# Kernel tuning notes

Hardware: AMD Instinct MI355X
Metric: run time of the kernel (lower is better)

## Reference

```python
import jax, jax.numpy as jnp
import numpy as np

N = 100_000
E = 1_600_000
F_IN, D1, D2, D_EMB = 64, 32, 64, 64
NUM_GRAPHS = 16
BN_EPS = 1e-5


def _glorot(key, shape):
    fan_in, fan_out = shape[0], shape[1]
    lim = (6.0 / (fan_in + fan_out)) ** 0.5
    return jax.random.uniform(key, shape, jnp.float32, -lim, lim)


def setup_inputs() -> dict:
    key = jax.random.key(0)
    ks = jax.random.split(key, 12)
    x = jax.random.normal(ks[0], (N, F_IN), jnp.float32)
    edge_index = jax.random.randint(ks[1], (2, E), 0, N, jnp.int64)
    batch = jnp.sort(jax.random.randint(ks[2], (N,), 0, NUM_GRAPHS, jnp.int64))
    return {
        "x": x,
        "edge_index": edge_index,
        "batch": batch,
        "num_graphs": NUM_GRAPHS,
        "num_nodes": N,
        "W1a": _glorot(ks[3], (F_IN, D1)), "b1a": jnp.zeros((D1,), jnp.float32),
        "W1b": _glorot(ks[4], (D1, D2)), "b1b": jnp.zeros((D2,), jnp.float32),
        "g1": jnp.ones((D2,), jnp.float32), "be1": jnp.zeros((D2,), jnp.float32),
        "W2a": _glorot(ks[5], (D2, D2)), "b2a": jnp.zeros((D2,), jnp.float32),
        "W2b": _glorot(ks[6], (D2, D_EMB)), "b2b": jnp.zeros((D_EMB,), jnp.float32),
        "g2": jnp.ones((D_EMB,), jnp.float32), "be2": jnp.zeros((D_EMB,), jnp.float32),
    }


def _batchnorm_train(h, gamma, beta):
    mean = jnp.mean(h, axis=0)
    var = jnp.mean(jnp.square(h - mean), axis=0)  # biased var, as torch BN uses for normalization
    return (h - mean) * jax.lax.rsqrt(var + BN_EPS) * gamma + beta


def _gin_aggregate(x, src, dst, valid, n_nodes):
    # sum_{j in N(i)} x_j over valid edges only (masked scatter-add)
    msg = x[src] * valid[:, None]  # [E, D]
    return jax.ops.segment_sum(msg, dst, num_segments=n_nodes)


def reference(x, edge_index, batch, num_graphs, num_nodes,
              W1a, b1a, W1b, b1b, g1, be1,
              W2a, b2a, W2b, b2b, g2, be2):
    n_edges = edge_index.shape[1]
    per = n_edges // num_graphs
    # edge_mask: per-edge threshold g * num_nodes / num_graphs applied to both rows
    thresh = jnp.repeat(jnp.arange(num_graphs), per).astype(jnp.float32) * (num_nodes / num_graphs)
    valid = jnp.all(edge_index.astype(jnp.float32) - thresh[None, :] >= 0.0, axis=0)
    valid = valid.astype(x.dtype)
    src, dst = edge_index[0], edge_index[1]

    # GINConv 1 (eps=0): nn1(x + aggr)
    h = x + _gin_aggregate(x, src, dst, valid, num_nodes)
    h = jax.nn.relu(h @ W1a + b1a) @ W1b + b1b
    h = jax.nn.relu(h)
    h = _batchnorm_train(h, g1, be1)

    # GINConv 2
    h = h + _gin_aggregate(h, src, dst, valid, num_nodes)
    h = jax.nn.relu(h @ W2a + b2a) @ W2b + b2b
    h = jax.nn.relu(h)
    h = _batchnorm_train(h, g2, be2)

    # global_mean_pool
    sums = jax.ops.segment_sum(h, batch, num_segments=num_graphs)
    counts = jax.ops.segment_sum(jnp.ones((h.shape[0],), h.dtype), batch, num_segments=num_graphs)
    return sums / jnp.maximum(counts, 1.0)[:, None]
```

## Files before the change

kernel.cpp:

```cpp
#include <hip/hip_runtime.h>
#include <hip/hip_fp16.h>

#define NG 16
#define D 64
#define SLOT 32
#define INP 68
#define NPB 64

union HF4 { float4 f4; __half2 h2[4]; };
union HF2 { float2 f2; __half2 h2[2]; };

__global__ void to_half_kernel(const float* __restrict__ in,
                               float2* __restrict__ out, int n4,
                               float4* __restrict__ xz,
                               float4* __restrict__ hz) {
  int t = blockIdx.x * 256 + threadIdx.x;
  if (blockIdx.x == 0 && threadIdx.x < 16) {
    float4 z = make_float4(0.f, 0.f, 0.f, 0.f);
    if (threadIdx.x < 8) xz[threadIdx.x] = z;
    else hz[threadIdx.x - 8] = z;
  }
  if (t < n4) {
    float4 v = ((const float4*)in)[t];
    HF2 u;
    u.h2[0] = __floats2half2_rn(v.x, v.y);
    u.h2[1] = __floats2half2_rn(v.z, v.w);
    out[t] = u.f2;
  }
}

__global__ void build_csr_kernel(const int* __restrict__ ei,
                                 int* __restrict__ fill,
                                 int* __restrict__ col,
                                 int E, int per, int tmul) {
  int e = blockIdx.x * blockDim.x + threadIdx.x;
  if (e >= E) return;
  int src = ei[e];
  int dst = ei[E + e];
  int g = e / per;
  int thr = g * tmul;
  if (src >= thr && dst >= thr) {
    int k = atomicAdd(&fill[dst], 1);
    if (k < SLOT) col[dst * SLOT + k] = src;
  }
}

__device__ __forceinline__ void tree_reduce_2x32(float* s_in, int tid) {
#pragma unroll
  for (int s = 16; s >= 1; s >>= 1) {
    if (tid < 32 * s) {
      int h = tid / (16 * s);
      int r = (tid / 16) % s;
      int qq = tid & 15;
      float4* a = (float4*)&s_in[(h * 32 + r) * INP + qq * 4];
      const float4 b = *(const float4*)&s_in[(h * 32 + r + s) * INP + qq * 4];
      a->x += b.x; a->y += b.y; a->z += b.z; a->w += b.w;
    }
    __syncthreads();
  }
}

template <int MID, bool FOLD_BN, int EPI>
__global__ __launch_bounds__(512, 2) void fused_layer_kernel(
    const float4* __restrict__ feat4,
    const int* __restrict__ col, const int* __restrict__ deg,
    const float* __restrict__ bn_sum, const float* __restrict__ bn_sq,
    const float* __restrict__ bn_gamma, const float* __restrict__ bn_beta,
    float invN,
    const float* __restrict__ Wa, const float* __restrict__ ba,
    const float* __restrict__ Wb, const float* __restrict__ bb,
    float2* __restrict__ out2,
    const int* __restrict__ batch,
    float* __restrict__ st_sum,
    float* __restrict__ st_sq,
    float* __restrict__ cnt,
    int N) {
  __shared__ float s_in[NPB * INP];
  __shared__ __half s_Wa[D * MID];
  __shared__ __half s_Wb[MID * D];
  __shared__ float s_bna[FOLD_BN ? D : 1];
  __shared__ float s_bnb[FOLD_BN ? D : 1];
  __shared__ int s_cnt[2];

  int tid = threadIdx.x;

  {
    const float4* wa4 = (const float4*)Wa;
    const float4* wb4 = (const float4*)Wb;
    __half2* sa2 = (__half2*)s_Wa;
    __half2* sb2 = (__half2*)s_Wb;
    constexpr int NW = D * MID / 4;
#pragma unroll
    for (int i = tid; i < NW; i += 512) {
      float4 a = wa4[i];
      float4 b = wb4[i];
      sa2[2 * i + 0] = __floats2half2_rn(a.x, a.y);
      sa2[2 * i + 1] = __floats2half2_rn(a.z, a.w);
      sb2[2 * i + 0] = __floats2half2_rn(b.x, b.y);
      sb2[2 * i + 1] = __floats2half2_rn(b.z, b.w);
    }
  }
  if (FOLD_BN && tid < D) {
    float mean = bn_sum[tid] * invN;
    float var = bn_sq[tid] * invN - mean * mean;
    float av = bn_gamma[tid] * rsqrtf(var + 1e-5f);
    s_bna[tid] = av;
    s_bnb[tid] = bn_beta[tid] - mean * av;
  }
  if (EPI == 2 && tid < 2) s_cnt[tid] = 0;
  __syncthreads();

  int base = blockIdx.x * NPB;

  {
    int slot = tid >> 3;
    int q8 = tid & 7;
    int node = base + slot;
    if (node < N) {
      int d = min(deg[node], SLOT);
      const int* cl = col + node * SLOT;
      float acc[8];
      {
        HF4 s; s.f4 = feat4[(size_t)node * 8 + q8];
#pragma unroll
        for (int i = 0; i < 4; i++) {
          float2 f = __half22float2(s.h2[i]);
          acc[2 * i] = f.x; acc[2 * i + 1] = f.y;
        }
      }
      int dpad = (d + 7) & ~7;
      for (int j = 0; j < dpad; j += 8) {
        int4 sa = *(const int4*)(cl + j);
        int4 sb = *(const int4*)(cl + j + 4);
        int i0 = (j + 0 < d) ? sa.x : N;
        int i1 = (j + 1 < d) ? sa.y : N;
        int i2 = (j + 2 < d) ? sa.z : N;
        int i3 = (j + 3 < d) ? sa.w : N;
        int i4 = (j + 4 < d) ? sb.x : N;
        int i5 = (j + 5 < d) ? sb.y : N;
        int i6 = (j + 6 < d) ? sb.z : N;
        int i7 = (j + 7 < d) ? sb.w : N;
        HF4 u0, u1, u2, u3, u4, u5, u6, u7;
        u0.f4 = feat4[(size_t)i0 * 8 + q8];
        u1.f4 = feat4[(size_t)i1 * 8 + q8];
        u2.f4 = feat4[(size_t)i2 * 8 + q8];
        u3.f4 = feat4[(size_t)i3 * 8 + q8];
        u4.f4 = feat4[(size_t)i4 * 8 + q8];
        u5.f4 = feat4[(size_t)i5 * 8 + q8];
        u6.f4 = feat4[(size_t)i6 * 8 + q8];
        u7.f4 = feat4[(size_t)i7 * 8 + q8];
#pragma unroll
        for (int i = 0; i < 4; i++) {
          float2 f0 = __half22float2(u0.h2[i]), f1 = __half22float2(u1.h2[i]);
          float2 f2 = __half22float2(u2.h2[i]), f3 = __half22float2(u3.h2[i]);
          float2 f4 = __half22float2(u4.h2[i]), f5 = __half22float2(u5.h2[i]);
          float2 f6 = __half22float2(u6.h2[i]), f7 = __half22float2(u7.h2[i]);
          acc[2 * i]     += (f0.x + f1.x + f2.x + f3.x) + (f4.x + f5.x + f6.x + f7.x);
          acc[2 * i + 1] += (f0.y + f1.y + f2.y + f3.y) + (f4.y + f5.y + f6.y + f7.y);
        }
      }
      if (FOLD_BN) {
        float dp = (float)(d + 1);
        int c = q8 * 8;
#pragma unroll
        for (int i = 0; i < 8; i++)
          acc[i] = s_bna[c + i] * acc[i] + dp * s_bnb[c + i];
      }
      *(float4*)&s_in[slot * INP + q8 * 8] =
          make_float4(acc[0], acc[1], acc[2], acc[3]);
      *(float4*)&s_in[slot * INP + q8 * 8 + 4] =
          make_float4(acc[4], acc[5], acc[6], acc[7]);
    }
  }
  __syncthreads();

  int q = tid & 15;
  int r2 = tid >> 4;
  int n0 = 2 * r2, n1 = n0 + 1;
  int node0 = base + n0, node1 = base + n1;
  constexpr int C1 = MID / 16;
  float4 o0, o1;
  {
    float acc0[C1], acc1[C1];
#pragma unroll
    for (int u = 0; u < C1; u++) { acc0[u] = ba[q * C1 + u]; acc1[u] = acc0[u]; }
#pragma unroll 4
    for (int j = 0; j < D; j++) {
      float v0 = s_in[n0 * INP + j];
      float v1 = s_in[n1 * INP + j];
      if constexpr (C1 == 2) {
        float2 w = __half22float2(((const __half2*)s_Wa)[j * 16 + q]);
        acc0[0] += v0 * w.x; acc0[1] += v0 * w.y;
        acc1[0] += v1 * w.x; acc1[1] += v1 * w.y;
      } else {
        HF2 u; u.f2 = ((const float2*)s_Wa)[j * 16 + q];
        float2 wA = __half22float2(u.h2[0]);
        float2 wB = __half22float2(u.h2[1]);
        acc0[0] += v0 * wA.x; acc0[1] += v0 * wA.y;
        acc0[2] += v0 * wB.x; acc0[3] += v0 * wB.y;
        acc1[0] += v1 * wA.x; acc1[1] += v1 * wA.y;
        acc1[2] += v1 * wB.x; acc1[3] += v1 * wB.y;
      }
    }
#pragma unroll
    for (int u = 0; u < C1; u++) {
      acc0[u] = fmaxf(acc0[u], 0.f);
      acc1[u] = fmaxf(acc1[u], 0.f);
    }

    o0 = *(const float4*)(bb + q * 4);
    o1 = o0;
#pragma unroll 8
    for (int k = 0; k < MID; k++) {
      float m0 = __shfl(acc0[k % C1], k / C1, 16);
      float m1 = __shfl(acc1[k % C1], k / C1, 16);
      HF2 u; u.f2 = ((const float2*)s_Wb)[k * 16 + q];
      float2 wA = __half22float2(u.h2[0]);
      float2 wB = __half22float2(u.h2[1]);
      o0.x += m0 * wA.x; o0.y += m0 * wA.y; o0.z += m0 * wB.x; o0.w += m0 * wB.y;
      o1.x += m1 * wA.x; o1.y += m1 * wA.y; o1.z += m1 * wB.x; o1.w += m1 * wB.y;
    }
    o0.x = fmaxf(o0.x, 0.f); o0.y = fmaxf(o0.y, 0.f);
    o0.z = fmaxf(o0.z, 0.f); o0.w = fmaxf(o0.w, 0.f);
    o1.x = fmaxf(o1.x, 0.f); o1.y = fmaxf(o1.y, 0.f);
    o1.z = fmaxf(o1.z, 0.f); o1.w = fmaxf(o1.w, 0.f);
    if (EPI == 1) {
      if (node0 < N) {
        HF2 u;
        u.h2[0] = __floats2half2_rn(o0.x, o0.y);
        u.h2[1] = __floats2half2_rn(o0.z, o0.w);
        out2[(size_t)node0 * 16 + q] = u.f2;
      }
      if (node1 < N) {
        HF2 u;
        u.h2[0] = __floats2half2_rn(o1.x, o1.y);
        u.h2[1] = __floats2half2_rn(o1.z, o1.w);
        out2[(size_t)node1 * 16 + q] = u.f2;
      }
    }
    if (node0 >= N) o0 = make_float4(0.f, 0.f, 0.f, 0.f);
    if (node1 >= N) o1 = make_float4(0.f, 0.f, 0.f, 0.f);
  }

  if (EPI == 1) {
    __syncthreads();
    *(float4*)&s_in[r2 * INP + q * 4] =
        make_float4(o0.x + o1.x, o0.y + o1.y, o0.z + o1.z, o0.w + o1.w);
    *(float4*)&s_in[(32 + r2) * INP + q * 4] =
        make_float4(o0.x * o0.x + o1.x * o1.x, o0.y * o0.y + o1.y * o1.y,
                    o0.z * o0.z + o1.z * o1.z, o0.w * o0.w + o1.w * o1.w);
    __syncthreads();
    tree_reduce_2x32(s_in, tid);
    if (tid < D) {
      atomicAdd(&st_sum[tid], s_in[tid]);
      atomicAdd(&st_sq[tid], s_in[32 * INP + tid]);
    }
  }

  if (EPI == 2) {
    int b0 = (node0 < N) ? batch[node0] : -1;
    int b1 = (node1 < N) ? batch[node1] : -1;
    int g_lo = batch[base];
    int g_hi = batch[min(base + NPB - 1, N - 1)];

    __syncthreads();
    if (q == 0) {
      atomicAdd(&s_cnt[0], (b0 == g_lo ? 1 : 0) + (b1 == g_lo ? 1 : 0));
      if (g_hi != g_lo)
        atomicAdd(&s_cnt[1], (b0 == g_hi ? 1 : 0) + (b1 == g_hi ? 1 : 0));
    }

    float w0 = (b0 == g_lo) ? 1.f : 0.f;
    float w1 = (b1 == g_lo) ? 1.f : 0.f;
    *(float4*)&s_in[r2 * INP + q * 4] =
        make_float4(w0 * o0.x + w1 * o1.x, w0 * o0.y + w1 * o1.y,
                    w0 * o0.z + w1 * o1.z, w0 * o0.w + w1 * o1.w);
    *(float4*)&s_in[(32 + r2) * INP + q * 4] =
        make_float4(o0.x * o0.x + o1.x * o1.x, o0.y * o0.y + o1.y * o1.y,
                    o0.z * o0.z + o1.z * o1.z, o0.w * o0.w + o1.w * o1.w);
    __syncthreads();
    tree_reduce_2x32(s_in, tid);
    if (tid < D) {
      atomicAdd(&st_sum[g_lo * D + tid], s_in[tid]);
      atomicAdd(&st_sq[tid], s_in[32 * INP + tid]);
    }
    if (tid == 0) atomicAdd(&cnt[g_lo], (float)s_cnt[0]);

    if (g_hi != g_lo) {
      __syncthreads();
      float u0 = (b0 == g_hi) ? 1.f : 0.f;
      float u1 = (b1 == g_hi) ? 1.f : 0.f;
      *(float4*)&s_in[r2 * INP + q * 4] =
          make_float4(u0 * o0.x + u1 * o1.x, u0 * o0.y + u1 * o1.y,
                      u0 * o0.z + u1 * o1.z, u0 * o0.w + u1 * o1.w);
      *(float4*)&s_in[(32 + r2) * INP + q * 4] = make_float4(0.f, 0.f, 0.f, 0.f);
      __syncthreads();
      tree_reduce_2x32(s_in, tid);
      if (tid < D) atomicAdd(&st_sum[g_hi * D + tid], s_in[tid]);
      if (tid == 0) atomicAdd(&cnt[g_hi], (float)s_cnt[1]);
    }
  }
}

__global__ void final_kernel(const float* __restrict__ pool,
                             const float* __restrict__ cnt,
                             const float* __restrict__ sq,
                             const float* __restrict__ gamma,
                             const float* __restrict__ beta,
                             float invN, float* __restrict__ out) {
  int c = threadIdx.x;
  float s = 0.f;
#pragma unroll
  for (int g = 0; g < NG; g++) s += pool[g * D + c];
  float mean = s * invN;
  float var = sq[c] * invN - mean * mean;
  float a = gamma[c] * rsqrtf(var + 1e-5f);
  float b = beta[c] - mean * a;
#pragma unroll
  for (int g = 0; g < NG; g++) {
    float n = cnt[g];
    out[g * D + c] = (a * pool[g * D + c] + n * b) / fmaxf(n, 1.f);
  }
}

extern "C" void kernel_launch(void* const* d_in, const int* in_sizes, int n_in,
                              void* d_out, int out_size, void* d_ws, size_t ws_size,
                              hipStream_t stream) {
  const float* x   = (const float*)d_in[0];
  const int* ei    = (const int*)d_in[1];
  const int* batch = (const int*)d_in[2];
  const float* W1a = (const float*)d_in[5];
  const float* b1a = (const float*)d_in[6];
  const float* W1b = (const float*)d_in[7];
  const float* b1b = (const float*)d_in[8];
  const float* g1  = (const float*)d_in[9];
  const float* be1 = (const float*)d_in[10];
  const float* W2a = (const float*)d_in[11];
  const float* b2a = (const float*)d_in[12];
  const float* W2b = (const float*)d_in[13];
  const float* b2b = (const float*)d_in[14];
  const float* g2  = (const float*)d_in[15];
  const float* be2 = (const float*)d_in[16];

  int N = in_sizes[0] / D;
  int E = in_sizes[1] / 2;
  int per = E / NG;
  int tmul = N / NG;
  float invN = 1.f / (float)N;

  float* ws = (float*)d_ws;
  size_t ndh = (size_t)(N + 1) * D / 2;
  float* h1h = ws;
  float* xh  = ws + ndh;
  int*   col = (int*)(ws + 2 * ndh);
  float* stats = ws + 2 * ndh + (size_t)N * SLOT;
  float* sum1 = stats;
  float* sq1  = stats + 64;
  float* pool = stats + 128;
  float* cnt  = stats + 128 + NG * D;
  float* sq2  = stats + 144 + NG * D;
  int*   fill = (int*)(stats + 208 + NG * D);

  hipMemsetAsync(stats, 0, (208 + NG * D + N) * sizeof(float), stream);

  int n4 = N * D / 4;
  to_half_kernel<<<(n4 + 255) / 256, 256, 0, stream>>>(
      x, (float2*)xh, n4,
      (float4*)(xh + (size_t)N * D / 2),
      (float4*)(h1h + (size_t)N * D / 2));

  build_csr_kernel<<<(E + 255) / 256, 256, 0, stream>>>(ei, fill, col, E, per, tmul);

  int fblocks = (N + NPB - 1) / NPB;

  fused_layer_kernel<32, false, 1><<<fblocks, 512, 0, stream>>>(
      (const float4*)xh, col, fill, nullptr, nullptr, nullptr, nullptr, invN,
      W1a, b1a, W1b, b1b, (float2*)h1h, nullptr, sum1, sq1, nullptr, N);

  fused_layer_kernel<64, true, 2><<<fblocks, 512, 0, stream>>>(
      (const float4*)h1h, col, fill, sum1, sq1, g1, be1, invN,
      W2a, b2a, W2b, b2b, nullptr, batch, pool, sq2, cnt, N);

  final_kernel<<<1, 64, 0, stream>>>(pool, cnt, sq2, g2, be2, invN, (float*)d_out);
}
```

Measured before the change: 264.3 us.

## Merge all stages into one persistent cooperative kernel with grid syncs

Replaces the memset, half conversion, CSR build, two fused layer kernels and the final kernel with a single cooperative launch that separates phases with grid.sync(). Blocks are persistent and loop over node tiles, and weights are staged into shared memory once per block per layer instead of once per tile. The goal is to remove per-launch overhead and the gaps between kernels. The cost is grid-wide barriers, a host-side occupancy query on every call, a grid limited to the resident block count, and shared memory now sized for the larger layer.

```diff
diff --git a/kernel.cpp b/kernel.cpp
--- a/kernel.cpp
+++ b/kernel.cpp
@@ -1,5 +1,8 @@
 #include <hip/hip_runtime.h>
 #include <hip/hip_fp16.h>
+#include <hip/hip_cooperative_groups.h>
+
+namespace cg = cooperative_groups;
 
 #define NG 16
 #define D 64
@@ -10,40 +13,19 @@
 union HF4 { float4 f4; __half2 h2[4]; };
 union HF2 { float2 f2; __half2 h2[2]; };
 
-__global__ void to_half_kernel(const float* __restrict__ in,
-                               float2* __restrict__ out, int n4,
-                               float4* __restrict__ xz,
-                               float4* __restrict__ hz) {
-  int t = blockIdx.x * 256 + threadIdx.x;
-  if (blockIdx.x == 0 && threadIdx.x < 16) {
-    float4 z = make_float4(0.f, 0.f, 0.f, 0.f);
-    if (threadIdx.x < 8) xz[threadIdx.x] = z;
-    else hz[threadIdx.x - 8] = z;
-  }
-  if (t < n4) {
-    float4 v = ((const float4*)in)[t];
-    HF2 u;
-    u.h2[0] = __floats2half2_rn(v.x, v.y);
-    u.h2[1] = __floats2half2_rn(v.z, v.w);
-    out[t] = u.f2;
-  }
-}
-
-__global__ void build_csr_kernel(const int* __restrict__ ei,
-                                 int* __restrict__ fill,
-                                 int* __restrict__ col,
-                                 int E, int per, int tmul) {
-  int e = blockIdx.x * blockDim.x + threadIdx.x;
-  if (e >= E) return;
-  int src = ei[e];
-  int dst = ei[E + e];
-  int g = e / per;
-  int thr = g * tmul;
-  if (src >= thr && dst >= thr) {
-    int k = atomicAdd(&fill[dst], 1);
-    if (k < SLOT) col[dst * SLOT + k] = src;
-  }
-}
+struct Params {
+  const float* x; const int* ei; const int* batch;
+  const float* W1a; const float* b1a; const float* W1b; const float* b1b;
+  const float* g1; const float* be1;
+  const float* W2a; const float* b2a; const float* W2b; const float* b2b;
+  const float* g2; const float* be2;
+  float* h1h; float* xh; int* col;
+  float* sum1; float* sq1; float* pool; float* cnt; float* sq2; int* fill;
+  int* zero_base; int zero_n;
+  float* out;
+  int N, E, per, tmul, n4, ntiles;
+  float invN;
+};
 
 __device__ __forceinline__ void tree_reduce_2x32(float* s_in, int tid) {
 #pragma unroll
@@ -60,57 +42,38 @@
   }
 }
 
+template <int MID>
+__device__ __forceinline__ void stage_weights(__half* s_Wa, __half* s_Wb,
+                                              const float* Wa, const float* Wb,
+                                              int tid) {
+  const float4* wa4 = (const float4*)Wa;
+  const float4* wb4 = (const float4*)Wb;
+  __half2* sa2 = (__half2*)s_Wa;
+  __half2* sb2 = (__half2*)s_Wb;
+  constexpr int NW = D * MID / 4;
+#pragma unroll
+  for (int i = tid; i < NW; i += 512) {
+    float4 a = wa4[i];
+    float4 b = wb4[i];
+    sa2[2 * i + 0] = __floats2half2_rn(a.x, a.y);
+    sa2[2 * i + 1] = __floats2half2_rn(a.z, a.w);
+    sb2[2 * i + 0] = __floats2half2_rn(b.x, b.y);
+    sb2[2 * i + 1] = __floats2half2_rn(b.z, b.w);
+  }
+}
+
 template <int MID, bool FOLD_BN, int EPI>
-__global__ __launch_bounds__(512, 2) void fused_layer_kernel(
-    const float4* __restrict__ feat4,
-    const int* __restrict__ col, const int* __restrict__ deg,
-    const float* __restrict__ bn_sum, const float* __restrict__ bn_sq,
-    const float* __restrict__ bn_gamma, const float* __restrict__ bn_beta,
-    float invN,
-    const float* __restrict__ Wa, const float* __restrict__ ba,
-    const float* __restrict__ Wb, const float* __restrict__ bb,
-    float2* __restrict__ out2,
-    const int* __restrict__ batch,
-    float* __restrict__ st_sum,
-    float* __restrict__ st_sq,
+__device__ __forceinline__ void layer_tile(
+    int base, int N, int tid,
+    const float4* __restrict__ feat4, const int* __restrict__ col,
+    const int* __restrict__ deg,
+    const float* __restrict__ ba, const float* __restrict__ bb,
+    float2* __restrict__ out2, const int* __restrict__ batch,
+    float* __restrict__ st_sum, float* __restrict__ st_sq,
     float* __restrict__ cnt,
-    int N) {
-  __shared__ float s_in[NPB * INP];
-  __shared__ __half s_Wa[D * MID];
-  __shared__ __half s_Wb[MID * D];
-  __shared__ float s_bna[FOLD_BN ? D : 1];
-  __shared__ float s_bnb[FOLD_BN ? D : 1];
-  __shared__ int s_cnt[2];
-
-  int tid = threadIdx.x;
-
-  {
-    const float4* wa4 = (const float4*)Wa;
-    const float4* wb4 = (const float4*)Wb;
-    __half2* sa2 = (__half2*)s_Wa;
-    __half2* sb2 = (__half2*)s_Wb;
-    constexpr int NW = D * MID / 4;
-#pragma unroll
-    for (int i = tid; i < NW; i += 512) {
-      float4 a = wa4[i];
-      float4 b = wb4[i];
-      sa2[2 * i + 0] = __floats2half2_rn(a.x, a.y);
-      sa2[2 * i + 1] = __floats2half2_rn(a.z, a.w);
-      sb2[2 * i + 0] = __floats2half2_rn(b.x, b.y);
-      sb2[2 * i + 1] = __floats2half2_rn(b.z, b.w);
-    }
-  }
-  if (FOLD_BN && tid < D) {
-    float mean = bn_sum[tid] * invN;
-    float var = bn_sq[tid] * invN - mean * mean;
-    float av = bn_gamma[tid] * rsqrtf(var + 1e-5f);
-    s_bna[tid] = av;
-    s_bnb[tid] = bn_beta[tid] - mean * av;
-  }
+    float* s_in, const __half* s_Wa, const __half* s_Wb,
+    const float* s_bna, const float* s_bnb, int* s_cnt) {
   if (EPI == 2 && tid < 2) s_cnt[tid] = 0;
-  __syncthreads();
-
-  int base = blockIdx.x * NPB;
 
   {
     int slot = tid >> 3;
@@ -302,84 +265,136 @@
   }
 }
 
-__global__ void final_kernel(const float* __restrict__ pool,
-                             const float* __restrict__ cnt,
-                             const float* __restrict__ sq,
-                             const float* __restrict__ gamma,
-                             const float* __restrict__ beta,
-                             float invN, float* __restrict__ out) {
-  int c = threadIdx.x;
-  float s = 0.f;
-#pragma unroll
-  for (int g = 0; g < NG; g++) s += pool[g * D + c];
-  float mean = s * invN;
-  float var = sq[c] * invN - mean * mean;
-  float a = gamma[c] * rsqrtf(var + 1e-5f);
-  float b = beta[c] - mean * a;
-#pragma unroll
-  for (int g = 0; g < NG; g++) {
-    float n = cnt[g];
-    out[g * D + c] = (a * pool[g * D + c] + n * b) / fmaxf(n, 1.f);
+__global__ __launch_bounds__(512, 2) void gin_coop_kernel(Params p) {
+  __shared__ float s_in[NPB * INP];
+  __shared__ __half s_Wa[D * D];
+  __shared__ __half s_Wb[D * D];
+  __shared__ float s_bna[D];
+  __shared__ float s_bnb[D];
+  __shared__ int s_cnt[2];
+
+  cg::grid_group grid = cg::this_grid();
+  int tid = threadIdx.x;
+  int gthread = blockIdx.x * 512 + tid;
+  int gstride = gridDim.x * 512;
+
+  for (int i = gthread; i < p.zero_n; i += gstride) p.zero_base[i] = 0;
+  for (int t = gthread; t < p.n4; t += gstride) {
+    float4 v = ((const float4*)p.x)[t];
+    HF2 u;
+    u.h2[0] = __floats2half2_rn(v.x, v.y);
+    u.h2[1] = __floats2half2_rn(v.z, v.w);
+    ((float2*)p.xh)[t] = u.f2;
+  }
+  if (gthread < 16) {
+    float4 z = make_float4(0.f, 0.f, 0.f, 0.f);
+    if (gthread < 8) ((float4*)(p.xh + (size_t)p.N * D / 2))[gthread] = z;
+    else ((float4*)(p.h1h + (size_t)p.N * D / 2))[gthread - 8] = z;
+  }
+  grid.sync();
+
+  for (int e = gthread; e < p.E; e += gstride) {
+    int src = p.ei[e];
+    int dst = p.ei[p.E + e];
+    int thr = (e / p.per) * p.tmul;
+    if (src >= thr && dst >= thr) {
+      int k = atomicAdd(&p.fill[dst], 1);
+      if (k < SLOT) p.col[dst * SLOT + k] = src;
+    }
+  }
+  grid.sync();
+
+  stage_weights<32>(s_Wa, s_Wb, p.W1a, p.W1b, tid);
+  __syncthreads();
+  for (int tile = blockIdx.x; tile < p.ntiles; tile += gridDim.x) {
+    layer_tile<32, false, 1>(tile * NPB, p.N, tid,
+        (const float4*)p.xh, p.col, p.fill, p.b1a, p.b1b,
+        (float2*)p.h1h, nullptr, p.sum1, p.sq1, nullptr,
+        s_in, s_Wa, s_Wb, s_bna, s_bnb, s_cnt);
+    __syncthreads();
+  }
+  grid.sync();
+
+  stage_weights<64>(s_Wa, s_Wb, p.W2a, p.W2b, tid);
+  if (tid < D) {
+    float mean = p.sum1[tid] * p.invN;
+    float var = p.sq1[tid] * p.invN - mean * mean;
+    float av = p.g1[tid] * rsqrtf(var + 1e-5f);
+    s_bna[tid] = av;
+    s_bnb[tid] = p.be1[tid] - mean * av;
+  }
+  __syncthreads();
+  for (int tile = blockIdx.x; tile < p.ntiles; tile += gridDim.x) {
+    layer_tile<64, true, 2>(tile * NPB, p.N, tid,
+        (const float4*)p.h1h, p.col, p.fill, p.b2a, p.b2b,
+        nullptr, p.batch, p.pool, p.sq2, p.cnt,
+        s_in, s_Wa, s_Wb, s_bna, s_bnb, s_cnt);
+    __syncthreads();
+  }
+  grid.sync();
+
+  if (blockIdx.x == 0 && tid < D) {
+    float s = 0.f;
+#pragma unroll
+    for (int g = 0; g < NG; g++) s += p.pool[g * D + tid];
+    float mean = s * p.invN;
+    float var = p.sq2[tid] * p.invN - mean * mean;
+    float a = p.g2[tid] * rsqrtf(var + 1e-5f);
+    float b = p.be2[tid] - mean * a;
+#pragma unroll
+    for (int g = 0; g < NG; g++) {
+      float n = p.cnt[g];
+      p.out[g * D + tid] = (a * p.pool[g * D + tid] + n * b) / fmaxf(n, 1.f);
+    }
   }
 }
 
 extern "C" void kernel_launch(void* const* d_in, const int* in_sizes, int n_in,
                               void* d_out, int out_size, void* d_ws, size_t ws_size,
                               hipStream_t stream) {
-  const float* x   = (const float*)d_in[0];
-  const int* ei    = (const int*)d_in[1];
-  const int* batch = (const int*)d_in[2];
-  const float* W1a = (const float*)d_in[5];
-  const float* b1a = (const float*)d_in[6];
-  const float* W1b = (const float*)d_in[7];
-  const float* b1b = (const float*)d_in[8];
-  const float* g1  = (const float*)d_in[9];
-  const float* be1 = (const float*)d_in[10];
-  const float* W2a = (const float*)d_in[11];
-  const float* b2a = (const float*)d_in[12];
-  const float* W2b = (const float*)d_in[13];
-  const float* b2b = (const float*)d_in[14];
-  const float* g2  = (const float*)d_in[15];
-  const float* be2 = (const float*)d_in[16];
-
-  int N = in_sizes[0] / D;
-  int E = in_sizes[1] / 2;
-  int per = E / NG;
-  int tmul = N / NG;
-  float invN = 1.f / (float)N;
+  Params p;
+  p.x   = (const float*)d_in[0];
+  p.ei  = (const int*)d_in[1];
+  p.batch = (const int*)d_in[2];
+  p.W1a = (const float*)d_in[5];  p.b1a = (const float*)d_in[6];
+  p.W1b = (const float*)d_in[7];  p.b1b = (const float*)d_in[8];
+  p.g1  = (const float*)d_in[9];  p.be1 = (const float*)d_in[10];
+  p.W2a = (const float*)d_in[11]; p.b2a = (const float*)d_in[12];
+  p.W2b = (const float*)d_in[13]; p.b2b = (const float*)d_in[14];
+  p.g2  = (const float*)d_in[15]; p.be2 = (const float*)d_in[16];
+
+  p.N = in_sizes[0] / D;
+  p.E = in_sizes[1] / 2;
+  p.per = p.E / NG;
+  p.tmul = p.N / NG;
+  p.n4 = p.N * D / 4;
+  p.ntiles = (p.N + NPB - 1) / NPB;
+  p.invN = 1.f / (float)p.N;
 
   float* ws = (float*)d_ws;
-  size_t ndh = (size_t)(N + 1) * D / 2;
-  float* h1h = ws;
-  float* xh  = ws + ndh;
-  int*   col = (int*)(ws + 2 * ndh);
-  float* stats = ws + 2 * ndh + (size_t)N * SLOT;
-  float* sum1 = stats;
-  float* sq1  = stats + 64;
-  float* pool = stats + 128;
-  float* cnt  = stats + 128 + NG * D;
-  float* sq2  = stats + 144 + NG * D;
-  int*   fill = (int*)(stats + 208 + NG * D);
-
-  hipMemsetAsync(stats, 0, (208 + NG * D + N) * sizeof(float), stream);
-
-  int n4 = N * D / 4;
-  to_half_kernel<<<(n4 + 255) / 256, 256, 0, stream>>>(
-      x, (float2*)xh, n4,
-      (float4*)(xh + (size_t)N * D / 2),
-      (float4*)(h1h + (size_t)N * D / 2));
-
-  build_csr_kernel<<<(E + 255) / 256, 256, 0, stream>>>(ei, fill, col, E, per, tmul);
-
-  int fblocks = (N + NPB - 1) / NPB;
-
-  fused_layer_kernel<32, false, 1><<<fblocks, 512, 0, stream>>>(
-      (const float4*)xh, col, fill, nullptr, nullptr, nullptr, nullptr, invN,
-      W1a, b1a, W1b, b1b, (float2*)h1h, nullptr, sum1, sq1, nullptr, N);
-
-  fused_layer_kernel<64, true, 2><<<fblocks, 512, 0, stream>>>(
-      (const float4*)h1h, col, fill, sum1, sq1, g1, be1, invN,
-      W2a, b2a, W2b, b2b, nullptr, batch, pool, sq2, cnt, N);
-
-  final_kernel<<<1, 64, 0, stream>>>(pool, cnt, sq2, g2, be2, invN, (float*)d_out);
+  size_t ndh = (size_t)(p.N + 1) * D / 2;
+  p.h1h = ws;
+  p.xh  = ws + ndh;
+  p.col = (int*)(ws + 2 * ndh);
+  float* stats = ws + 2 * ndh + (size_t)p.N * SLOT;
+  p.sum1 = stats;
+  p.sq1  = stats + 64;
+  p.pool = stats + 128;
+  p.cnt  = stats + 128 + NG * D;
+  p.sq2  = stats + 144 + NG * D;
+  p.fill = (int*)(stats + 208 + NG * D);
+  p.zero_base = (int*)stats;
+  p.zero_n = 208 + NG * D + p.N;
+  p.out = (float*)d_out;
+
+  int bpc = 0;
+  hipOccupancyMaxActiveBlocksPerMultiprocessor(
+      &bpc, reinterpret_cast<const void*>(gin_coop_kernel), 512, 0);
+  if (bpc < 1) bpc = 1;
+  int G = bpc * 256;
+  if (G > p.ntiles) G = p.ntiles;
+
+  void* args[] = { &p };
+  hipLaunchCooperativeKernel(reinterpret_cast<void*>(gin_coop_kernel),
+                             dim3(G), dim3(512), args, 0, stream);
 }
```

After: 434.0 us. 64.2% more time.
